# Optimization experiments

Measured on AMD Instinct MI355X. Metric: run time of the kernel, lower is better.

## Reference

```python
import jax, jax.numpy as jnp
import numpy as np

D_MODEL = 1024
H = 16
D_HEAD = D_MODEL // H  # 64


def setup_inputs() -> dict:
    key = jax.random.key(0)
    ks = jax.random.split(key, 11)
    B, L = 4, 1024
    s = 0.02
    return {
        "Q": jax.random.normal(ks[0], (B, L, D_MODEL), jnp.float32),
        "K": jax.random.normal(ks[1], (B, L, D_MODEL), jnp.float32),
        "V": jax.random.normal(ks[2], (B, L, D_MODEL), jnp.float32),
        # per-head Dense weights stacked on a leading head axis (Keras Dense: y = x @ W + b)
        "Wq": jax.random.normal(ks[3], (H, D_MODEL, D_HEAD), jnp.float32) * s,
        "bq": jnp.zeros((H, D_HEAD), jnp.float32),
        "Wk": jax.random.normal(ks[4], (H, D_MODEL, D_HEAD), jnp.float32) * s,
        "bk": jnp.zeros((H, D_HEAD), jnp.float32),
        "Wv": jax.random.normal(ks[5], (H, D_MODEL, D_HEAD), jnp.float32) * s,
        "bv": jnp.zeros((H, D_HEAD), jnp.float32),
        "Wo": jax.random.normal(ks[6], (D_MODEL, D_MODEL), jnp.float32) * s,
        "bo": jnp.zeros((D_MODEL,), jnp.float32),
    }


def reference(Q, K, V, Wq, bq, Wk, bk, Wv, bv, Wo, bo):
    # per-head projections, vectorized over heads: [B, H, L, Dh]
    q = jnp.einsum("bld,hde->bhle", Q, Wq) + bq[None, :, None, :]
    k = jnp.einsum("bld,hde->bhle", K, Wk) + bk[None, :, None, :]
    v = jnp.einsum("bld,hde->bhle", V, Wv) + bv[None, :, None, :]
    # scaled dot-product attention scores: [B, H, Lq, Lk]
    scores = jnp.einsum("bhqe,bhke->bhqk", q, k) / jnp.sqrt(jnp.asarray(D_HEAD, q.dtype))
    attn = jax.nn.softmax(scores, axis=-1)
    out_h = jnp.einsum("bhqk,bhke->bhqe", attn, v)  # [B, H, Lq, Dh]
    # concat heads along feature dim (matches tf.concat(heads, axis=2))
    B, Hh, Lq, Dh = out_h.shape
    concat = out_h.transpose(0, 2, 1, 3).reshape(B, Lq, Hh * Dh)
    output = concat @ Wo + bo
    # tf.stack(heads_attention) -> [H, B, Lq, Lk]
    attention = attn.transpose(1, 0, 2, 3)
    return output, attention
```

## Files before the change

### kernel.cpp

```cpp
#include <hip/hip_runtime.h>
#include <stdint.h>

#define DEVI __device__ __forceinline__
typedef unsigned short u16;
typedef __attribute__((ext_vector_type(8))) short s16x8;
typedef __attribute__((ext_vector_type(4))) float f32x4;

typedef __attribute__((address_space(1))) void as1_void;
typedef __attribute__((address_space(3))) void as3_void;

DEVI u16 f2b(float f){
  union { float f; uint32_t u; } x; x.f = f;
  return (u16)((x.u + 0x7fffu + ((x.u >> 16) & 1u)) >> 16);
}
DEVI float b2f(u16 u){
  union { uint32_t u; float f; } x; x.u = ((uint32_t)u) << 16;
  return x.f;
}
DEVI void gload16(const void* g, void* l){
  __builtin_amdgcn_global_load_lds((as1_void*)g, (as3_void*)l, 16, 0, 0);
}
DEVI f32x4 MFMA(s16x8 a, s16x8 b, f32x4 c){
  return __builtin_amdgcn_mfma_f32_16x16x32_bf16(a, b, c, 0, 0, 0);
}

__global__ __launch_bounds__(256)
void k_prep(const float* __restrict__ Q, const float* __restrict__ Kc,
            const float* __restrict__ V,
            u16* __restrict__ Qb, u16* __restrict__ Kb, u16* __restrict__ Vb,
            const float* __restrict__ Wq, const float* __restrict__ Wk,
            const float* __restrict__ Wv, const float* __restrict__ Wo,
            u16* __restrict__ WqT, u16* __restrict__ WkT,
            u16* __restrict__ WvT, u16* __restrict__ WoT){
  __shared__ float t[64][65];
  const int bid = blockIdx.x, tid = threadIdx.x;
  if(bid < 12288){
    int tno = bid >> 12;
    int blk = bid & 4095;
    const float* s = (tno == 0) ? Q : (tno == 1) ? Kc : V;
    u16* d = (tno == 0) ? Qb : (tno == 1) ? Kb : Vb;
    int i = (blk * 256 + tid) * 4;
    float4 v = *(const float4*)(s + i);
    ushort4 o;
    o.x = f2b(v.x); o.y = f2b(v.y); o.z = f2b(v.z); o.w = f2b(v.w);
    *(ushort4*)(d + i) = o;
  } else {
    int j = bid - 12288;
    const float* src; u16* dst; int C, r0, c0;
    if(j < 768){
      int tno = j >> 8, rem = j & 255, head = rem >> 4, rt = rem & 15;
      src = ((tno == 0) ? Wq : (tno == 1) ? Wk : Wv) + head * 65536;
      dst = ((tno == 0) ? WqT : (tno == 1) ? WkT : WvT) + head * 65536;
      C = 64; r0 = rt * 64; c0 = 0;
    } else {
      int j2 = j - 768;
      src = Wo; dst = WoT; C = 1024;
      r0 = (j2 & 15) * 64; c0 = (j2 >> 4) * 64;
    }
    int tx = tid & 63, ty = tid >> 6;
    #pragma unroll
    for(int i2 = 0; i2 < 64; i2 += 4)
      t[ty + i2][tx] = src[(size_t)(r0 + ty + i2) * C + c0 + tx];
    __syncthreads();
    #pragma unroll
    for(int i2 = 0; i2 < 64; i2 += 4)
      dst[(size_t)(c0 + ty + i2) * 1024 + r0 + tx] = f2b(t[tx][ty + i2]);
  }
}

template<int BM, int BK>
DEVI void gemm_core(int mode, const u16* __restrict__ A, const u16* __restrict__ Bt,
                    const float* __restrict__ bias, void* __restrict__ Cp,
                    int m0, int n0, u16* sAb, u16* sBb){
  const int tid = threadIdx.x, w = tid >> 6, l = tid & 63;
  const int wr = w >> 1, wc = w & 1;
  constexpr int MI = BM / 32;
  constexpr int KK = BK / 32;
  constexpr int CPR = BK / 8;
  constexpr int CPT_A = BM * BK / 2048;
  constexpr int CPT_B = 128 * BK / 2048;
  constexpr int RB = 2 * BK;
  f32x4 acc[MI][4];
  #pragma unroll
  for(int a = 0; a < MI; a++)
    #pragma unroll
    for(int b = 0; b < 4; b++) acc[a][b] = (f32x4){0.f, 0.f, 0.f, 0.f};

  const int NT = 1024 / BK;
  auto STAGE = [&](int buf, int t){
    #pragma unroll
    for(int s2 = 0; s2 < CPT_A; s2++){
      int c = s2 * 256 + tid;
      int r = c / CPR, ch = (c % CPR) ^ (r & (CPR - 1));
      gload16((const char*)A + ((size_t)(m0 + r) * 1024 + t * BK) * 2 + ch * 16,
              (char*)sAb + (size_t)buf * BM * RB + c * 16);
    }
    #pragma unroll
    for(int s2 = 0; s2 < CPT_B; s2++){
      int c = s2 * 256 + tid;
      int r = c / CPR, ch = (c % CPR) ^ (r & (CPR - 1));
      gload16((const char*)Bt + ((size_t)(n0 + r) * 1024 + t * BK) * 2 + ch * 16,
              (char*)sBb + (size_t)buf * 128 * RB + c * 16);
    }
  };
  STAGE(0, 0);
  __syncthreads();
  for(int t = 0; t < NT; t++){
    const int cur = t & 1;
    if(t + 1 < NT) STAGE(cur ^ 1, t + 1);
    const char* pa = (const char*)sAb + (size_t)cur * BM * RB;
    const char* pb = (const char*)sBb + (size_t)cur * 128 * RB;
    s16x8 af[MI][KK], bf[4][KK];
    #pragma unroll
    for(int mi = 0; mi < MI; mi++){
      int r = (BM / 2) * wr + 16 * mi + (l & 15);
      #pragma unroll
      for(int kk = 0; kk < KK; kk++)
        af[mi][kk] = *(const s16x8*)(pa + r * RB +
                     ((kk * 64 + 16 * (l >> 4)) ^ ((r & (CPR - 1)) << 4)));
    }
    #pragma unroll
    for(int ni = 0; ni < 4; ni++){
      int r = 64 * wc + 16 * ni + (l & 15);
      #pragma unroll
      for(int kk = 0; kk < KK; kk++)
        bf[ni][kk] = *(const s16x8*)(pb + r * RB +
                     ((kk * 64 + 16 * (l >> 4)) ^ ((r & (CPR - 1)) << 4)));
    }
    #pragma unroll
    for(int kk = 0; kk < KK; kk++)
      #pragma unroll
      for(int mi = 0; mi < MI; mi++)
        #pragma unroll
        for(int ni = 0; ni < 4; ni++)
          acc[mi][ni] = MFMA(af[mi][kk], bf[ni][kk], acc[mi][ni]);
    __syncthreads();
  }
  #pragma unroll
  for(int mi = 0; mi < MI; mi++){
    #pragma unroll
    for(int ni = 0; ni < 4; ni++){
      #pragma unroll
      for(int i = 0; i < 4; i++){
        int gr = m0 + (BM / 2) * wr + 16 * mi + 4 * (l >> 4) + i;
        int gc = n0 + 64 * wc + 16 * ni + (l & 15);
        float v = acc[mi][ni][i];
        if(mode == 0){
          ((u16*)Cp)[(size_t)gr * 1024 + gc] = f2b(v + bias[gc]);
        } else if(mode == 1){
          ((u16*)Cp)[((size_t)(gc >> 10) << 20) + ((size_t)gr << 10) + (gc & 1023)] =
              f2b(v + bias[gr]);
        } else {
          ((float*)Cp)[(size_t)gr * 1024 + gc] = v + bias[gc];
        }
      }
    }
  }
}

__global__ __launch_bounds__(256, 3)
void k_proj(const u16* __restrict__ Qb, const u16* __restrict__ Kb,
            const u16* __restrict__ Vb,
            const u16* __restrict__ WqT, const u16* __restrict__ WkT,
            const u16* __restrict__ WvT,
            const float* __restrict__ bq, const float* __restrict__ bk,
            const float* __restrict__ bv,
            u16* __restrict__ q_ws, u16* __restrict__ k_ws, u16* __restrict__ vT_ws){
  __shared__ u16 sA[2][128 * 32];
  __shared__ u16 sB[2][128 * 32];
  const int raw = blockIdx.x;
  const int bid = (raw & 7) * 96 + (raw >> 3);
  if(bid < 256){
    gemm_core<128, 32>(0, Qb, WqT, bq, q_ws, (bid >> 3) * 128, (bid & 7) * 128,
                       &sA[0][0], &sB[0][0]);
  } else if(bid < 512){
    int b2 = bid - 256;
    gemm_core<128, 32>(0, Kb, WkT, bk, k_ws, (b2 >> 3) * 128, (b2 & 7) * 128,
                       &sA[0][0], &sB[0][0]);
  } else {
    int b2 = bid - 512;
    gemm_core<128, 32>(1, WvT, Vb, bv, vT_ws, (b2 >> 5) * 128, (b2 & 31) * 128,
                       &sA[0][0], &sB[0][0]);
  }
}

__global__ __launch_bounds__(256)
void k_final(const u16* __restrict__ A, const u16* __restrict__ Bt,
             const float* __restrict__ bias, float* __restrict__ C){
  __shared__ u16 sA[2][64 * 64];
  __shared__ u16 sB[2][128 * 64];
  const int raw = blockIdx.x;
  const int bid = (raw & 7) * 64 + (raw >> 3);
  gemm_core<64, 64>(2, A, Bt, bias, C, (bid >> 3) * 64, (bid & 7) * 128,
                    &sA[0][0], &sB[0][0]);
}

__global__ __launch_bounds__(256)
void k_attn(const u16* __restrict__ qws, const u16* __restrict__ kws,
            const u16* __restrict__ vws, float* __restrict__ attn,
            u16* __restrict__ concat){
  __shared__ u16 q_s[64 * 64];
  __shared__ u16 k_s[128 * 64];
  __shared__ u16 v_s[64 * 128];
  __shared__ u16 p_s[64 * 128];
  const int tid = threadIdx.x, w = tid >> 6, l = tid & 63;
  const int bx = blockIdx.x;
  const int bh = bx & 63, qb = bx >> 6, b = bh >> 4, h = bh & 15;
  const char* qg = (const char*)qws + ((size_t)(b * 1024 + qb * 64) * 1024 + h * 64) * 2;
  const char* kg = (const char*)kws + ((size_t)(b * 1024) * 1024 + h * 64) * 2;
  const char* vg = (const char*)vws + ((size_t)b * 1048576 + (size_t)h * 64 * 1024) * 2;
  float* ao = attn + (size_t)((h * 4 + b) * 1024 + qb * 64) * 1024;
  u16* cw = concat + (size_t)(b * 1024 + qb * 64) * 1024 + h * 64;

  #pragma unroll
  for(int s2 = 0; s2 < 2; s2++){
    int s = 2 * w + s2;
    int r = s * 8 + (l >> 3);
    int ch = (l & 7) ^ (r & 7);
    gload16(qg + (size_t)r * 2048 + ch * 16, (char*)q_s + s * 1024 + l * 16);
  }

  const float KS = 0.18033688011112042f;
  float rs[4] = {0.f, 0.f, 0.f, 0.f};
  s16x8 af0, af1;

  for(int kt = 0; kt < 8; kt++){
    __syncthreads();
    #pragma unroll
    for(int s2 = 0; s2 < 4; s2++){
      int s = 4 * w + s2;
      int r = s * 8 + (l >> 3);
      int ch = (l & 7) ^ (r & 7);
      gload16(kg + (size_t)(kt * 128 + r) * 2048 + ch * 16, (char*)k_s + s * 1024 + l * 16);
    }
    __syncthreads();
    if(kt == 0){
      int rq = 16 * w + (l & 15);
      af0 = *(const s16x8*)((const char*)q_s + rq * 128 + ((16 * (l >> 4)) ^ ((rq & 7) << 4)));
      af1 = *(const s16x8*)((const char*)q_s + rq * 128 + ((64 + 16 * (l >> 4)) ^ ((rq & 7) << 4)));
    }
    #pragma unroll
    for(int f = 0; f < 8; f++){
      int r = 16 * f + (l & 15);
      s16x8 b0 = *(const s16x8*)((const char*)k_s + r * 128 + ((16 * (l >> 4)) ^ ((r & 7) << 4)));
      s16x8 b1 = *(const s16x8*)((const char*)k_s + r * 128 + ((64 + 16 * (l >> 4)) ^ ((r & 7) << 4)));
      f32x4 sf = (f32x4){0.f, 0.f, 0.f, 0.f};
      sf = MFMA(af0, b0, sf);
      sf = MFMA(af1, b1, sf);
      #pragma unroll
      for(int i = 0; i < 4; i++) rs[i] += exp2f(sf[i] * KS);
    }
  }
  #pragma unroll
  for(int i = 0; i < 4; i++){
    #pragma unroll
    for(int m = 1; m < 16; m <<= 1) rs[i] += __shfl_xor(rs[i], m, 64);
  }
  float inv[4];
  #pragma unroll
  for(int i = 0; i < 4; i++) inv[i] = 1.0f / rs[i];

  f32x4 oacc[4];
  #pragma unroll
  for(int fe = 0; fe < 4; fe++) oacc[fe] = (f32x4){0.f, 0.f, 0.f, 0.f};

  for(int kt = 0; kt < 8; kt++){
    __syncthreads();
    #pragma unroll
    for(int s2 = 0; s2 < 4; s2++){
      int s = 4 * w + s2;
      int r = s * 8 + (l >> 3);
      int ch = (l & 7) ^ (r & 7);
      gload16(kg + (size_t)(kt * 128 + r) * 2048 + ch * 16, (char*)k_s + s * 1024 + l * 16);
    }
    #pragma unroll
    for(int s2 = 0; s2 < 4; s2++){
      int s = 4 * w + s2;
      int e = s * 4 + (l >> 4);
      int ch = (l & 15) ^ (e & 15);
      gload16(vg + (size_t)e * 2048 + (size_t)kt * 256 + ch * 16, (char*)v_s + s * 1024 + l * 16);
    }
    __syncthreads();
    f32x4 sf[8];
    #pragma unroll
    for(int f = 0; f < 8; f++){
      int r = 16 * f + (l & 15);
      s16x8 b0 = *(const s16x8*)((const char*)k_s + r * 128 + ((16 * (l >> 4)) ^ ((r & 7) << 4)));
      s16x8 b1 = *(const s16x8*)((const char*)k_s + r * 128 + ((64 + 16 * (l >> 4)) ^ ((r & 7) << 4)));
      sf[f] = (f32x4){0.f, 0.f, 0.f, 0.f};
      sf[f] = MFMA(af0, b0, sf[f]);
      sf[f] = MFMA(af1, b1, sf[f]);
    }
    #pragma unroll
    for(int f = 0; f < 8; f++){
      #pragma unroll
      for(int i = 0; i < 4; i++){
        float p = exp2f(sf[f][i] * KS) * inv[i];
        int rr = 16 * w + 4 * (l >> 4) + i;
        *(u16*)((char*)p_s + rr * 256 + (((16 * f + (l & 15)) * 2) ^ ((rr & 15) << 4))) = f2b(p);
      }
    }
    __syncthreads();
    #pragma unroll
    for(int kc = 0; kc < 4; kc++){
      int rp = 16 * w + (l & 15);
      s16x8 pa = *(const s16x8*)((const char*)p_s + rp * 256 + ((kc * 64 + 16 * (l >> 4)) ^ ((rp & 15) << 4)));
      #pragma unroll
      for(int fe = 0; fe < 4; fe++){
        int e = 16 * fe + (l & 15);
        s16x8 bv = *(const s16x8*)((const char*)v_s + e * 256 + ((kc * 64 + 16 * (l >> 4)) ^ ((e & 15) << 4)));
        oacc[fe] = MFMA(pa, bv, oacc[fe]);
      }
    }
    #pragma unroll
    for(int it = 0; it < 8; it++){
      int row = 16 * w + 2 * it + (l >> 5);
      int cb = 8 * (l & 31);
      uint2 pv = *(const uint2*)((const char*)p_s + row * 256 +
                                 (cb ^ ((row & 15) << 4)));
      f32x4 o;
      o[0] = b2f((u16)(pv.x & 0xffffu));
      o[1] = b2f((u16)(pv.x >> 16));
      o[2] = b2f((u16)(pv.y & 0xffffu));
      o[3] = b2f((u16)(pv.y >> 16));
      __builtin_nontemporal_store(
          o, (f32x4*)(ao + (size_t)row * 1024 + kt * 128 + (l & 31) * 4));
    }
  }
  #pragma unroll
  for(int fe = 0; fe < 4; fe++){
    #pragma unroll
    for(int i = 0; i < 4; i++){
      int qi = 16 * w + 4 * (l >> 4) + i;
      cw[(size_t)qi * 1024 + 16 * fe + (l & 15)] = f2b(oacc[fe][i]);
    }
  }
}

extern "C" void kernel_launch(void* const* d_in, const int* in_sizes, int n_in,
                              void* d_out, int out_size, void* d_ws, size_t ws_size,
                              hipStream_t stream){
  const float* Q  = (const float*)d_in[0];
  const float* Kc = (const float*)d_in[1];
  const float* V  = (const float*)d_in[2];
  const float* Wq = (const float*)d_in[3];
  const float* bq = (const float*)d_in[4];
  const float* Wk = (const float*)d_in[5];
  const float* bk = (const float*)d_in[6];
  const float* Wv = (const float*)d_in[7];
  const float* bv = (const float*)d_in[8];
  const float* Wo = (const float*)d_in[9];
  const float* bo = (const float*)d_in[10];
  float* out = (float*)d_out;

  char* ws = (char*)d_ws;
  u16* q_ws      = (u16*)(ws + 0);
  u16* k_ws      = (u16*)(ws + 8388608);
  u16* vT_ws     = (u16*)(ws + 16777216);
  u16* concat_ws = (u16*)(ws + 25165824);
  u16* WqT = (u16*)(ws + 33554432);
  u16* WkT = (u16*)(ws + 35651584);
  u16* WvT = (u16*)(ws + 37748736);
  u16* WoT = (u16*)(ws + 39845888);

  u16* Qb = (u16*)((char*)d_out + 16777216);
  u16* Kb = (u16*)((char*)d_out + 25165824);
  u16* Vb = (u16*)((char*)d_out + 33554432);
  float* attn = out + 4194304;

  k_prep<<<13312, 256, 0, stream>>>(Q, Kc, V, Qb, Kb, Vb,
                                    Wq, Wk, Wv, Wo, WqT, WkT, WvT, WoT);
  k_proj<<<768, 256, 0, stream>>>(Qb, Kb, Vb, WqT, WkT, WvT, bq, bk, bv,
                                  q_ws, k_ws, vT_ws);
  k_attn<<<1024, 256, 0, stream>>>(q_ws, k_ws, vT_ws, attn, concat_ws);
  k_final<<<512, 256, 0, stream>>>(concat_ws, WoT, bo, out);
}
```

Before: 166.4 us.

## Double-buffer K/V tiles in attention kernel with smaller 64-key tiles

The attention kernel now uses 64-key tiles with double-buffered K and V shared-memory stages, so the next tile's async global-to-LDS loads run while the current tile is computed. Q fragments are read straight from global memory into registers, which removes the Q staging buffer. Shared memory drops and launch_bounds asks for 4 blocks per CU to raise occupancy. P is written and read within a wave's own rows, so one barrier per tile is removed. The cost is twice as many loop iterations, and the tighter register budget could cause spills.

```diff
diff --git a/kernel.cpp b/kernel.cpp
--- a/kernel.cpp
+++ b/kernel.cpp
@@ -195,14 +195,13 @@
                     &sA[0][0], &sB[0][0]);
 }
 
-__global__ __launch_bounds__(256)
+__global__ __launch_bounds__(256, 4)
 void k_attn(const u16* __restrict__ qws, const u16* __restrict__ kws,
             const u16* __restrict__ vws, float* __restrict__ attn,
             u16* __restrict__ concat){
-  __shared__ u16 q_s[64 * 64];
-  __shared__ u16 k_s[128 * 64];
-  __shared__ u16 v_s[64 * 128];
-  __shared__ u16 p_s[64 * 128];
+  __shared__ u16 k_s[2][64 * 64];
+  __shared__ u16 v_s[2][64 * 64];
+  __shared__ u16 p_s[64 * 64];
   const int tid = threadIdx.x, w = tid >> 6, l = tid & 63;
   const int bx = blockIdx.x;
   const int bh = bx & 63, qb = bx >> 6, b = bh >> 4, h = bh & 15;
@@ -212,44 +211,52 @@
   float* ao = attn + (size_t)((h * 4 + b) * 1024 + qb * 64) * 1024;
   u16* cw = concat + (size_t)(b * 1024 + qb * 64) * 1024 + h * 64;
 
-  #pragma unroll
-  for(int s2 = 0; s2 < 2; s2++){
-    int s = 2 * w + s2;
-    int r = s * 8 + (l >> 3);
-    int ch = (l & 7) ^ (r & 7);
-    gload16(qg + (size_t)r * 2048 + ch * 16, (char*)q_s + s * 1024 + l * 16);
+  auto STAGEK = [&](int buf, int kt){
+    #pragma unroll
+    for(int rd = 0; rd < 2; rd++){
+      int c = rd * 256 + tid;
+      int r = c >> 3, ch = c & 7;
+      gload16(kg + (size_t)(kt * 64 + r) * 2048 + ((ch ^ (r & 7)) * 16),
+              (char*)k_s[buf] + c * 16);
+    }
+  };
+  auto STAGEV = [&](int buf, int kt){
+    #pragma unroll
+    for(int rd = 0; rd < 2; rd++){
+      int c = rd * 256 + tid;
+      int e = c >> 3, ch = c & 7;
+      gload16(vg + (size_t)e * 2048 + kt * 128 + ((ch ^ (e & 7)) * 16),
+              (char*)v_s[buf] + c * 16);
+    }
+  };
+
+  s16x8 af0, af1;
+  {
+    int rq = 16 * w + (l & 15);
+    af0 = *(const s16x8*)(qg + (size_t)rq * 2048 + (l >> 4) * 16);
+    af1 = *(const s16x8*)(qg + (size_t)rq * 2048 + 64 + (l >> 4) * 16);
   }
 
   const float KS = 0.18033688011112042f;
   float rs[4] = {0.f, 0.f, 0.f, 0.f};
-  s16x8 af0, af1;
-
-  for(int kt = 0; kt < 8; kt++){
-    __syncthreads();
-    #pragma unroll
-    for(int s2 = 0; s2 < 4; s2++){
-      int s = 4 * w + s2;
-      int r = s * 8 + (l >> 3);
-      int ch = (l & 7) ^ (r & 7);
-      gload16(kg + (size_t)(kt * 128 + r) * 2048 + ch * 16, (char*)k_s + s * 1024 + l * 16);
-    }
-    __syncthreads();
-    if(kt == 0){
-      int rq = 16 * w + (l & 15);
-      af0 = *(const s16x8*)((const char*)q_s + rq * 128 + ((16 * (l >> 4)) ^ ((rq & 7) << 4)));
-      af1 = *(const s16x8*)((const char*)q_s + rq * 128 + ((64 + 16 * (l >> 4)) ^ ((rq & 7) << 4)));
-    }
-    #pragma unroll
-    for(int f = 0; f < 8; f++){
+
+  STAGEK(0, 0);
+  __syncthreads();
+  for(int kt = 0; kt < 16; kt++){
+    const int cur = kt & 1;
+    if(kt + 1 < 16) STAGEK(cur ^ 1, kt + 1);
+    #pragma unroll
+    for(int f = 0; f < 4; f++){
       int r = 16 * f + (l & 15);
-      s16x8 b0 = *(const s16x8*)((const char*)k_s + r * 128 + ((16 * (l >> 4)) ^ ((r & 7) << 4)));
-      s16x8 b1 = *(const s16x8*)((const char*)k_s + r * 128 + ((64 + 16 * (l >> 4)) ^ ((r & 7) << 4)));
+      s16x8 b0 = *(const s16x8*)((const char*)k_s[cur] + r * 128 + ((16 * (l >> 4)) ^ ((r & 7) << 4)));
+      s16x8 b1 = *(const s16x8*)((const char*)k_s[cur] + r * 128 + ((64 + 16 * (l >> 4)) ^ ((r & 7) << 4)));
       f32x4 sf = (f32x4){0.f, 0.f, 0.f, 0.f};
       sf = MFMA(af0, b0, sf);
       sf = MFMA(af1, b1, sf);
       #pragma unroll
       for(int i = 0; i < 4; i++) rs[i] += exp2f(sf[i] * KS);
     }
+    __syncthreads();
   }
   #pragma unroll
   for(int i = 0; i < 4; i++){
@@ -264,68 +271,59 @@
   #pragma unroll
   for(int fe = 0; fe < 4; fe++) oacc[fe] = (f32x4){0.f, 0.f, 0.f, 0.f};
 
-  for(int kt = 0; kt < 8; kt++){
-    __syncthreads();
-    #pragma unroll
-    for(int s2 = 0; s2 < 4; s2++){
-      int s = 4 * w + s2;
-      int r = s * 8 + (l >> 3);
-      int ch = (l & 7) ^ (r & 7);
-      gload16(kg + (size_t)(kt * 128 + r) * 2048 + ch * 16, (char*)k_s + s * 1024 + l * 16);
-    }
-    #pragma unroll
-    for(int s2 = 0; s2 < 4; s2++){
-      int s = 4 * w + s2;
-      int e = s * 4 + (l >> 4);
-      int ch = (l & 15) ^ (e & 15);
-      gload16(vg + (size_t)e * 2048 + (size_t)kt * 256 + ch * 16, (char*)v_s + s * 1024 + l * 16);
-    }
-    __syncthreads();
-    f32x4 sf[8];
-    #pragma unroll
-    for(int f = 0; f < 8; f++){
+  STAGEK(0, 0);
+  STAGEV(0, 0);
+  __syncthreads();
+  for(int kt = 0; kt < 16; kt++){
+    const int cur = kt & 1;
+    if(kt + 1 < 16){ STAGEK(cur ^ 1, kt + 1); STAGEV(cur ^ 1, kt + 1); }
+    f32x4 sf[4];
+    #pragma unroll
+    for(int f = 0; f < 4; f++){
       int r = 16 * f + (l & 15);
-      s16x8 b0 = *(const s16x8*)((const char*)k_s + r * 128 + ((16 * (l >> 4)) ^ ((r & 7) << 4)));
-      s16x8 b1 = *(const s16x8*)((const char*)k_s + r * 128 + ((64 + 16 * (l >> 4)) ^ ((r & 7) << 4)));
+      s16x8 b0 = *(const s16x8*)((const char*)k_s[cur] + r * 128 + ((16 * (l >> 4)) ^ ((r & 7) << 4)));
+      s16x8 b1 = *(const s16x8*)((const char*)k_s[cur] + r * 128 + ((64 + 16 * (l >> 4)) ^ ((r & 7) << 4)));
       sf[f] = (f32x4){0.f, 0.f, 0.f, 0.f};
       sf[f] = MFMA(af0, b0, sf[f]);
       sf[f] = MFMA(af1, b1, sf[f]);
     }
     #pragma unroll
-    for(int f = 0; f < 8; f++){
+    for(int f = 0; f < 4; f++){
       #pragma unroll
       for(int i = 0; i < 4; i++){
         float p = exp2f(sf[f][i] * KS) * inv[i];
         int rr = 16 * w + 4 * (l >> 4) + i;
-        *(u16*)((char*)p_s + rr * 256 + (((16 * f + (l & 15)) * 2) ^ ((rr & 15) << 4))) = f2b(p);
+        int cc = 16 * f + (l & 15);
+        *(u16*)((char*)p_s + rr * 128 + ((cc * 2) ^ ((rr & 7) << 4))) = f2b(p);
       }
     }
-    __syncthreads();
-    #pragma unroll
-    for(int kc = 0; kc < 4; kc++){
+    #pragma unroll
+    for(int kc = 0; kc < 2; kc++){
       int rp = 16 * w + (l & 15);
-      s16x8 pa = *(const s16x8*)((const char*)p_s + rp * 256 + ((kc * 64 + 16 * (l >> 4)) ^ ((rp & 15) << 4)));
+      s16x8 pa = *(const s16x8*)((const char*)p_s + rp * 128 +
+                  ((kc * 64 + 16 * (l >> 4)) ^ ((rp & 7) << 4)));
       #pragma unroll
       for(int fe = 0; fe < 4; fe++){
         int e = 16 * fe + (l & 15);
-        s16x8 bv = *(const s16x8*)((const char*)v_s + e * 256 + ((kc * 64 + 16 * (l >> 4)) ^ ((e & 15) << 4)));
+        s16x8 bv = *(const s16x8*)((const char*)v_s[cur] + e * 128 +
+                    ((kc * 64 + 16 * (l >> 4)) ^ ((e & 7) << 4)));
         oacc[fe] = MFMA(pa, bv, oacc[fe]);
       }
     }
     #pragma unroll
-    for(int it = 0; it < 8; it++){
-      int row = 16 * w + 2 * it + (l >> 5);
-      int cb = 8 * (l & 31);
-      uint2 pv = *(const uint2*)((const char*)p_s + row * 256 +
-                                 (cb ^ ((row & 15) << 4)));
+    for(int it = 0; it < 4; it++){
+      int row = 16 * w + 4 * it + (l >> 4);
+      uint2 pv = *(const uint2*)((const char*)p_s + row * 128 +
+                                 ((8 * (l & 15)) ^ ((row & 7) << 4)));
       f32x4 o;
       o[0] = b2f((u16)(pv.x & 0xffffu));
       o[1] = b2f((u16)(pv.x >> 16));
       o[2] = b2f((u16)(pv.y & 0xffffu));
       o[3] = b2f((u16)(pv.y >> 16));
       __builtin_nontemporal_store(
-          o, (f32x4*)(ao + (size_t)row * 1024 + kt * 128 + (l & 31) * 4));
-    }
+          o, (f32x4*)(ao + (size_t)row * 1024 + kt * 64 + (l & 15) * 4));
+    }
+    __syncthreads();
   }
   #pragma unroll
   for(int fe = 0; fe < 4; fe++){
```

Result: faster. 160.6 us (-3.5%).
